# Kernel optimization log

Hardware: AMD Instinct MI355X
Metric: run time of the kernel (lower is better)

Reference implementation:

```python
import jax, jax.numpy as jnp
import numpy as np

N, T, H, L, E, F, CN, CG = 20000, 2, 128, 4, 320000, 514, 3, 2
EPS = 1e-7  # GENConv message epsilon


def _ln(x, g, b):
    mu = jnp.mean(x, axis=-1, keepdims=True)
    var = jnp.mean((x - mu) ** 2, axis=-1, keepdims=True)
    return (x - mu) / jnp.sqrt(var + 1e-5) * g + b


def _genconv(x, src, dst, e, W1, b1, g1, be1, W2, b2, t, n):
    # message: relu(x_j + edge_attr) + eps
    msg = jax.nn.relu(x[src] + e) + EPS  # [E,H]
    # softmax aggregation with learnable temperature t, grouped by dst
    logits = msg * t
    m = jax.ops.segment_max(logits, dst, num_segments=n)
    m = jnp.where(jnp.isfinite(m), m, 0.0)  # guard empty segments
    ex = jnp.exp(logits - m[dst])
    denom = jax.ops.segment_sum(ex, dst, num_segments=n)
    alpha = ex / (denom[dst] + 1e-16)
    agg = jax.ops.segment_sum(msg * alpha, dst, num_segments=n)  # [N,H]
    out = agg + x  # residual with root node (x_r)
    # MLP: Lin(H,2H) -> LayerNorm -> ReLU -> Lin(2H,H)
    h1 = jax.nn.relu(_ln(out @ W1 + b1, g1, be1))
    return h1 @ W2 + b2


def _attn(x, Wq, Wk, Wv, gamma):
    # x: [N, T, H]; channel (transform-axis) self-attention, gamma-gated residual
    q = jnp.einsum('tc,nch->nth', Wq, x)
    k = jnp.einsum('tc,nch->nth', Wk, x)
    v = jnp.einsum('tc,nch->nth', Wv, x)
    a = jax.nn.softmax(jnp.einsum('nth,nsh->nts', q, k), axis=-1)
    o = jnp.einsum('nts,nsh->nth', a, v)
    return gamma * o + x


def setup_inputs() -> dict:
    key = jax.random.key(0)
    ks = iter(jax.random.split(key, 48))

    def nrm(sh, s=0.02):
        return jax.random.normal(next(ks), sh, dtype=jnp.float32) * s

    inp = {}
    inp['node_feature'] = jax.random.normal(next(ks), (N, F), dtype=jnp.float32)
    inp['edge_index'] = jax.random.randint(next(ks), (T, 2, E), 0, N, dtype=jnp.int32)
    inp['edge_attr'] = jax.random.normal(next(ks), (T, E, 2), dtype=jnp.float32)
    # encoders
    inp['Wne'] = nrm((F, H)); inp['bne'] = jnp.zeros((H,), jnp.float32)
    inp['Wee'] = nrm((2, H)); inp['bee'] = jnp.zeros((H,), jnp.float32)
    # per-layer GENConv MLP params (stacked over L)
    inp['W1'] = nrm((L, H, 2 * H)); inp['b1'] = jnp.zeros((L, 2 * H), jnp.float32)
    inp['g1'] = jnp.ones((L, 2 * H), jnp.float32); inp['be1'] = jnp.zeros((L, 2 * H), jnp.float32)
    inp['W2'] = nrm((L, 2 * H, H)); inp['b2'] = jnp.zeros((L, H), jnp.float32)
    # DeepGCNLayer LayerNorms
    inp['dg'] = jnp.ones((L, H), jnp.float32); inp['db'] = jnp.zeros((L, H), jnp.float32)
    # learnable temperatures
    inp['t'] = jnp.ones((L,), jnp.float32)
    # node attention + head
    inp['Wq_n'] = nrm((T, T), 0.2); inp['Wk_n'] = nrm((T, T), 0.2); inp['Wv_n'] = nrm((T, T), 0.2)
    inp['gamma_n'] = jnp.float32(0.5)
    inp['Wn1'] = nrm((T * H, T * H)); inp['bn1'] = jnp.zeros((T * H,), jnp.float32)
    inp['Wn2'] = nrm((T * H, CN)); inp['bn2'] = jnp.zeros((CN,), jnp.float32)
    # graph attention + head
    inp['Wq_g'] = nrm((T, T), 0.2); inp['Wk_g'] = nrm((T, T), 0.2); inp['Wv_g'] = nrm((T, T), 0.2)
    inp['gamma_g'] = jnp.float32(0.5)
    inp['Wg1'] = nrm((T * H, T * H)); inp['bg1'] = jnp.zeros((T * H,), jnp.float32)
    inp['Wg2'] = nrm((T * H, CG)); inp['bg2'] = jnp.zeros((CG,), jnp.float32)
    return inp


def reference(node_feature, edge_index, edge_attr, Wne, bne, Wee, bee,
              W1, b1, g1, be1, W2, b2, dg, db, t,
              Wq_n, Wk_n, Wv_n, gamma_n, Wn1, bn1, Wn2, bn2,
              Wq_g, Wk_g, Wv_g, gamma_g, Wg1, bg1, Wg2, bg2):
    embs = []
    for ti in range(T):
        x = node_feature @ Wne + bne           # node_encoder
        e = edge_attr[ti] @ Wee + bee          # edge_encoder
        src, dst = edge_index[ti, 0], edge_index[ti, 1]
        # layers[0].conv applied directly
        x = _genconv(x, src, dst, e, W1[0], b1[0], g1[0], be1[0], W2[0], b2[0], t[0], N)
        # res+ DeepGCN blocks
        for l in range(1, L):
            h = jax.nn.relu(_ln(x, dg[l], db[l]))  # dropout p=0.1 is identity in eval
            x = x + _genconv(h, src, dst, e, W1[l], b1[l], g1[l], be1[l], W2[l], b2[l], t[l], N)
        x = jax.nn.relu(_ln(x, dg[0], db[0]))
        embs.append(x)
    emb = jnp.stack(embs, axis=1)  # [N, T, H]

    a = _attn(emb, Wq_n, Wk_n, Wv_n, gamma_n).reshape(N, T * H)
    node = jax.nn.relu(a @ Wn1 + bn1) @ Wn2 + bn2
    node = jax.nn.log_softmax(node, axis=-1)

    g = _attn(emb, Wq_g, Wk_g, Wv_g, gamma_g).reshape(N, T * H)
    gp = jnp.mean(g, axis=0, keepdims=True)  # global_mean_pool (single graph)
    gp = jax.nn.relu(gp @ Wg1 + bg1) @ Wg2 + bg2
    gp = jax.nn.log_softmax(gp, axis=-1)
    return (node, gp)
```

## Files before the change

### kernel.cpp

```cpp
#include <hip/hip_runtime.h>

#define NN 20000
#define TT 2
#define HH 128
#define LL 4
#define EE 320000
#define FF 514
#define CN 3
#define CG 2
#define MP 20096

typedef __bf16 bf16x8 __attribute__((ext_vector_type(8)));
typedef __bf16 bf16x4 __attribute__((ext_vector_type(4)));
typedef __bf16 bf16x2 __attribute__((ext_vector_type(2)));
typedef float f32x4 __attribute__((ext_vector_type(4)));

struct __align__(8) Edge { int src; __bf16 ea0, ea1; };

__device__ inline float wave_sum(float v) {
#pragma unroll
  for (int off = 32; off; off >>= 1) v += __shfl_xor(v, off);
  return v;
}
__device__ inline float red16(float v) {
  v += __shfl_xor(v, 1); v += __shfl_xor(v, 2);
  v += __shfl_xor(v, 4); v += __shfl_xor(v, 8);
  return v;
}

__device__ __forceinline__ float fexp2(float x) {
#if __has_builtin(__builtin_amdgcn_exp2f)
  return __builtin_amdgcn_exp2f(x);
#else
  return exp2f(x);
#endif
}

__device__ __forceinline__ void gload_lds16(const void* g, void* l) {
  __builtin_amdgcn_global_load_lds(
      (const __attribute__((address_space(1))) unsigned int*)g,
      (__attribute__((address_space(3))) unsigned int*)l, 16, 0, 0);
}

#define ENCB (MP / 64)
#define SSB 313
#define CHUNK 5000
__global__ __launch_bounds__(256) void enc_scatter_kernel(
    const __bf16* __restrict__ A, const __bf16* __restrict__ BT,
    const float* __restrict__ bias, __bf16* __restrict__ C,
    const int* __restrict__ edge_index, const float* __restrict__ edge_attr,
    int* __restrict__ cursor, Edge* __restrict__ edges) {
  __shared__ __bf16 As[2][64][32];
  __shared__ __bf16 Bs[2][128][32];
  const int tid = threadIdx.x;
  if (blockIdx.x >= ENCB) {
    int sb = blockIdx.x - ENCB;
    int chunk = sb & 7;
    int slice = sb >> 3;
    int i0 = slice * 2048 + tid * 8;
    if (i0 >= 2 * EE) return;
    int ti = (i0 >= EE) ? 1 : 0;
    int e0 = i0 - ti * EE;
    const int* srcp = edge_index + (size_t)ti * 2 * EE;
    int dst8[8];
    __builtin_memcpy(dst8, srcp + EE + e0, 32);
#pragma unroll
    for (int j = 0; j < 8; ++j) {
      int gnode = ti * NN + dst8[j];
      if (gnode / CHUNK != chunk) continue;
      int s = srcp[e0 + j];
      float2 ea = ((const float2*)edge_attr)[(size_t)ti * EE + e0 + j];
      int pos = atomicAdd(&cursor[gnode], 1);
      Edge ed;
      ed.src = s + ti * MP;
      ed.ea0 = (__bf16)ea.x; ed.ea1 = (__bf16)ea.y;
      __builtin_memcpy(&edges[pos], &ed, sizeof(Edge));
    }
    return;
  }
  const int K = 576;
  const int lane = tid & 63, w = tid >> 6;
  const int bm = blockIdx.x * 64;
  const int wr = (w >> 1) * 32, wc = (w & 1) * 64;
  const int fr = lane & 15, fq = lane >> 4;
  const int rowA = tid >> 2, chA = (tid & 3) * 8;
  const __bf16* Ab = A + (size_t)(bm + rowA) * K + chA;
  const __bf16* Bb = BT + (size_t)rowA * K + chA;
  const __bf16* Bb2 = Bb + (size_t)64 * K;
  f32x4 acc[2][4] = {};
#define STAGE(buf, k0)                                  \
  do {                                                  \
    gload_lds16(Ab + (k0), &As[buf][rowA][chA]);        \
    gload_lds16(Bb + (k0), &Bs[buf][rowA][chA]);        \
    gload_lds16(Bb2 + (k0), &Bs[buf][rowA + 64][chA]);  \
  } while (0)
  STAGE(0, 0);
  __syncthreads();
  int cur = 0;
  for (int k0 = 0; k0 < K; k0 += 32) {
    if (k0 + 32 < K) STAGE(cur ^ 1, k0 + 32);
    bf16x8 af[2], bq[4];
#pragma unroll
    for (int m = 0; m < 2; ++m)
      af[m] = *(const bf16x8*)&As[cur][wr + m * 16 + fr][fq * 8];
#pragma unroll
    for (int n = 0; n < 4; ++n)
      bq[n] = *(const bf16x8*)&Bs[cur][wc + n * 16 + fr][fq * 8];
#pragma unroll
    for (int m = 0; m < 2; ++m)
#pragma unroll
      for (int n = 0; n < 4; ++n)
        acc[m][n] =
            __builtin_amdgcn_mfma_f32_16x16x32_bf16(af[m], bq[n], acc[m][n], 0, 0, 0);
    __syncthreads();
    cur ^= 1;
  }
#undef STAGE
#pragma unroll
  for (int m = 0; m < 2; ++m) {
#pragma unroll
    for (int n = 0; n < 4; ++n) {
#pragma unroll
      for (int j = 0; j < 4; ++j) {
        int gm = bm + wr + m * 16 + fq * 4 + j;
        int gn = wc + n * 16 + fr;
        if (gm < NN) {
          __bf16 c = (__bf16)(acc[m][n][j] + bias[gn]);
          C[(size_t)gm * 128 + gn] = c;
          C[(size_t)(gm + MP) * 128 + gn] = c;
        }
      }
    }
  }
}

template <int EPI>
__global__ __launch_bounds__(256) void gemm256(
    const __bf16* __restrict__ A, const __bf16* __restrict__ BT,
    const float* __restrict__ bias, const float* __restrict__ g,
    const float* __restrict__ be, const float* __restrict__ W2h,
    const float* __restrict__ b2h, void* __restrict__ outp, int M, int K) {
  __shared__ __bf16 As[2][64][32];
  __shared__ __bf16 Bs[2][256][32];
  const int tid = threadIdx.x;
  const int lane = tid & 63, w = tid >> 6;
  const int bm = blockIdx.x * 64;
  const int wr = w * 16;
  const int fr = lane & 15, fq = lane >> 4;
  const int rowA = tid >> 2, chA = (tid & 3) * 8;
  const __bf16* Ab = A + (size_t)(bm + rowA) * K + chA;
  const __bf16* Bb = BT + (size_t)rowA * K + chA;
  f32x4 acc[16] = {};

#define STG(buf, k0)                                                \
  do {                                                              \
    gload_lds16(Ab + (k0), &As[buf][rowA][chA]);                    \
    _Pragma("unroll") for (int r = 0; r < 4; ++r)                   \
        gload_lds16(Bb + (size_t)(r * 64) * K + (k0),               \
                    &Bs[buf][rowA + r * 64][chA]);                  \
  } while (0)

  STG(0, 0);
  __syncthreads();
  int cur = 0;
  for (int k0 = 0; k0 < K; k0 += 32) {
    if (k0 + 32 < K) STG(cur ^ 1, k0 + 32);
    bf16x8 af = *(const bf16x8*)&As[cur][wr + fr][fq * 8];
#pragma unroll
    for (int n = 0; n < 16; ++n) {
      bf16x8 bq = *(const bf16x8*)&Bs[cur][n * 16 + fr][fq * 8];
      acc[n] = __builtin_amdgcn_mfma_f32_16x16x32_bf16(af, bq, acc[n], 0, 0, 0);
    }
    __syncthreads();
    cur ^= 1;
  }
#undef STG

  float cb[16];
#pragma unroll
  for (int n = 0; n < 16; ++n) cb[n] = bias[n * 16 + fr];

  if constexpr (EPI == 0) {
    float gv[16], bev[16];
#pragma unroll
    for (int n = 0; n < 16; ++n) {
      gv[n] = g[n * 16 + fr];
      bev[n] = be[n * 16 + fr];
    }
    __bf16* outb = (__bf16*)outp;
#pragma unroll
    for (int j = 0; j < 4; ++j) {
      float cj[16], s = 0.f, s2 = 0.f;
#pragma unroll
      for (int n = 0; n < 16; ++n) {
        float c = acc[n][j] + cb[n];
        cj[n] = c; s += c; s2 += c * c;
      }
      s = red16(s); s2 = red16(s2);
      float mu = s * (1.f / 256);
      float var = fmaxf(s2 * (1.f / 256) - mu * mu, 0.f);
      float rr = rsqrtf(var + 1e-5f);
      int gm = bm + wr + fq * 4 + j;
      __bf16* op = outb + (size_t)gm * 256;
#pragma unroll
      for (int n = 0; n < 16; ++n) {
        float y = (cj[n] - mu) * rr * gv[n] + bev[n];
        op[n * 16 + fr] = (__bf16)fmaxf(y, 0.f);
      }
    }
  } else {
    float w0[16], w1[16], w2[16];
#pragma unroll
    for (int n = 0; n < 16; ++n) {
      int col = n * 16 + fr;
      w0[n] = W2h[col * 3 + 0];
      w1[n] = W2h[col * 3 + 1];
      w2[n] = W2h[col * 3 + 2];
    }
    float* outf = (float*)outp;
#pragma unroll
    for (int j = 0; j < 4; ++j) {
      float p0 = 0.f, p1 = 0.f, p2 = 0.f;
#pragma unroll
      for (int n = 0; n < 16; ++n) {
        float h = fmaxf(acc[n][j] + cb[n], 0.f);
        p0 += h * w0[n]; p1 += h * w1[n]; p2 += h * w2[n];
      }
      p0 = red16(p0); p1 = red16(p1); p2 = red16(p2);
      int gm = bm + wr + fq * 4 + j;
      if (fr == 0 && gm < M) {
        float l0 = p0 + b2h[0], l1 = p1 + b2h[1], l2 = p2 + b2h[2];
        float m = fmaxf(l0, fmaxf(l1, l2));
        float lse = m + logf(__expf(l0 - m) + __expf(l1 - m) + __expf(l2 - m));
        outf[(size_t)gm * 3 + 0] = l0 - lse;
        outf[(size_t)gm * 3 + 1] = l1 - lse;
        outf[(size_t)gm * 3 + 2] = l2 - lse;
      }
    }
  }
}

template <int MODE>
__global__ __launch_bounds__(256) void gemm_lin2(
    const __bf16* __restrict__ A, const __bf16* __restrict__ BT,
    const float* __restrict__ bias, float* __restrict__ xres,
    const float* __restrict__ g, const float* __restrict__ be,
    void* __restrict__ lnout) {
  __shared__ __bf16 As[2][64][32];
  __shared__ __bf16 Bs[2][128][32];
  __shared__ float redS[64][2], redS2[64][2];
  const int tid = threadIdx.x;
  const int lane = tid & 63, w = tid >> 6;
  const int bm = blockIdx.x * 64;
  const int wr = (w >> 1) * 32, wc = (w & 1) * 64;
  const int fr = lane & 15, fq = lane >> 4;
  const int rowA = tid >> 2, chA = (tid & 3) * 8;
  const __bf16* Ab = A + (size_t)(bm + rowA) * 256 + chA;
  const __bf16* Bb = BT + (size_t)rowA * 256 + chA;
  const __bf16* Bb2 = Bb + (size_t)64 * 256;
  f32x4 acc[2][4] = {};

#define STAGE(buf, k0)                                  \
  do {                                                  \
    gload_lds16(Ab + (k0), &As[buf][rowA][chA]);        \
    gload_lds16(Bb + (k0), &Bs[buf][rowA][chA]);        \
    gload_lds16(Bb2 + (k0), &Bs[buf][rowA + 64][chA]);  \
  } while (0)

  STAGE(0, 0);
  __syncthreads();
  int cur = 0;
  for (int k0 = 0; k0 < 256; k0 += 32) {
    if (k0 + 32 < 256) STAGE(cur ^ 1, k0 + 32);
    bf16x8 af[2], bq[4];
#pragma unroll
    for (int m = 0; m < 2; ++m)
      af[m] = *(const bf16x8*)&As[cur][wr + m * 16 + fr][fq * 8];
#pragma unroll
    for (int n = 0; n < 4; ++n)
      bq[n] = *(const bf16x8*)&Bs[cur][wc + n * 16 + fr][fq * 8];
#pragma unroll
    for (int m = 0; m < 2; ++m)
#pragma unroll
      for (int n = 0; n < 4; ++n)
        acc[m][n] =
            __builtin_amdgcn_mfma_f32_16x16x32_bf16(af[m], bq[n], acc[m][n], 0, 0, 0);
    __syncthreads();
    cur ^= 1;
  }
#undef STAGE

  float cv[2][4][4];
#pragma unroll
  for (int m = 0; m < 2; ++m) {
    int r0 = wr + m * 16 + fq * 4;
#pragma unroll
    for (int j = 0; j < 4; ++j) {
      int gm = bm + r0 + j;
      float s = 0.f, s2 = 0.f;
#pragma unroll
      for (int n = 0; n < 4; ++n) {
        float c = acc[m][n][j] + bias[wc + n * 16 + fr];
        if (MODE != 0) c += xres[(size_t)gm * 128 + wc + n * 16 + fr];
        cv[m][n][j] = c;
        s += c; s2 += c * c;
      }
      s = red16(s); s2 = red16(s2);
      if (fr == 0) {
        redS[r0 + j][w & 1] = s;
        redS2[r0 + j][w & 1] = s2;
      }
    }
  }
  __syncthreads();
#pragma unroll
  for (int m = 0; m < 2; ++m) {
    int r0 = wr + m * 16 + fq * 4;
#pragma unroll
    for (int j = 0; j < 4; ++j) {
      int r = r0 + j;
      int gm = bm + r;
      float S = redS[r][0] + redS[r][1];
      float S2 = redS2[r][0] + redS2[r][1];
      float mu = S * (1.f / 128);
      float var = fmaxf(S2 * (1.f / 128) - mu * mu, 0.f);
      float rr = rsqrtf(var + 1e-5f);
      if constexpr (MODE < 2) {
        float* xp = xres + (size_t)gm * 128;
        __bf16* hp = (__bf16*)lnout + (size_t)gm * 128;
#pragma unroll
        for (int n = 0; n < 4; ++n) {
          int col = wc + n * 16 + fr;
          float c = cv[m][n][j];
          xp[col] = c;
          float y = (c - mu) * rr * g[col] + be[col];
          hp[col] = (__bf16)fmaxf(y, 0.f);
        }
      } else {
        int half = gm >= MP;
        int node = gm - half * MP;
        if (node < NN) {
          float* ep = (float*)lnout + (size_t)node * 256 + half * 128;
#pragma unroll
          for (int n = 0; n < 4; ++n) {
            int col = wc + n * 16 + fr;
            float y = (cv[m][n][j] - mu) * rr * g[col] + be[col];
            ep[col] = fmaxf(y, 0.f);
          }
        }
      }
    }
  }
}

struct WtDesc { const float* src; __bf16* dst; int K, N, Kpad, gbase; };
struct WtDescs { WtDesc d[10]; };
#define NFG 1440000
#define WTG 50176
#define CTG 80000
#define PREPG 2048

__global__ __launch_bounds__(256) void prep_kernel(
    const float* __restrict__ nf_src, __bf16* __restrict__ nf_dst, WtDescs descs,
    const int* __restrict__ edge_index, int* __restrict__ deg,
    float* __restrict__ gp_sum) {
  const int tid = threadIdx.x;
  if (blockIdx.x == 0) gp_sum[tid] = 0.f;
  const int TOT = NFG + WTG + CTG;
  for (int g = blockIdx.x * 256 + tid; g < TOT; g += PREPG * 256) {
    if (g < NFG) {
      int row = g / 72, colg = g - row * 72;
      int col0 = colg * 8;
      bf16x8 o;
      if (col0 + 8 <= FF) {
        float v[8];
        __builtin_memcpy(v, nf_src + (size_t)row * FF + col0, 32);
#pragma unroll
        for (int i = 0; i < 8; ++i) o[i] = (__bf16)v[i];
      } else {
#pragma unroll
        for (int i = 0; i < 8; ++i) {
          int col = col0 + i;
          o[i] = (__bf16)((col < FF) ? nf_src[(size_t)row * FF + col] : 0.f);
        }
      }
      *(bf16x8*)(nf_dst + (size_t)row * 576 + col0) = o;
    } else if (g < NFG + WTG) {
      int wb = g - NFG;
      int di = 0;
#pragma unroll
      for (int t = 1; t < 10; ++t)
        if (wb >= descs.d[t].gbase) di = t;
      WtDesc de = descs.d[di];
      int local = wb - de.gbase;
      int kg8 = de.Kpad >> 3;
      int n = local / kg8, k0 = (local - n * kg8) * 8;
      bf16x8 o;
#pragma unroll
      for (int i = 0; i < 8; ++i) {
        int k = k0 + i;
        o[i] = (__bf16)((k < de.K) ? de.src[(size_t)k * de.N + n] : 0.f);
      }
      *(bf16x8*)(de.dst + (size_t)n * de.Kpad + k0) = o;
    } else {
      int i0 = (g - NFG - WTG) * 8;
      int ti = (i0 >= EE) ? 1 : 0;
      int e0 = i0 - ti * EE;
      int dst8[8];
      __builtin_memcpy(dst8, edge_index + (size_t)ti * 2 * EE + EE + e0, 32);
      int* dbase = deg + ti * NN;
#pragma unroll
      for (int j = 0; j < 8; ++j) atomicAdd(&dbase[dst8[j]], 1);
    }
  }
}

__global__ __launch_bounds__(1024) void scan2_kernel(
    const int* __restrict__ deg_all, int* __restrict__ rowptr,
    int* __restrict__ cursor) {
  const int ti = blockIdx.x;
  const int* deg = deg_all + ti * NN;
  __shared__ int sums[1024];
  int tid = threadIdx.x;
  int chunk = (NN + 1023) / 1024;
  int begin = tid * chunk, end = min(begin + chunk, NN);
  int s = 0;
  for (int i = begin; i < end; ++i) s += deg[i];
  sums[tid] = s;
  __syncthreads();
  for (int off = 1; off < 1024; off <<= 1) {
    int v = (tid >= off) ? sums[tid - off] : 0;
    __syncthreads();
    sums[tid] += v;
    __syncthreads();
  }
  int running = ti * EE + sums[tid] - s;
  for (int i = begin; i < end; ++i) {
    rowptr[ti * NN + i] = running;
    cursor[ti * NN + i] = running;
    running += deg[i];
  }
  if (tid == 0 && ti == 1) rowptr[2 * NN] = 2 * EE;
}

__global__ __launch_bounds__(256) void agg_kernel(
    const __bf16* __restrict__ xin, const int* __restrict__ rowptr,
    const Edge* __restrict__ edges, const float* __restrict__ Wee,
    const float* __restrict__ bee, const float* __restrict__ tptr, int layer,
    __bf16* __restrict__ out) {
  int wave = threadIdx.x >> 6, lane = threadIdx.x & 63;
  int b = blockIdx.x;
  int x8 = b & 7;
  int q = x8 >> 1;
  int par = x8 & 1;
  int ti = q >> 1, chh = q & 1;
  int group = (b >> 3) * 2 + par;
  int qq = lane >> 4, c15 = lane & 15;
  int node = group * 16 + wave * 4 + qq;
  int gnode = ti * NN + node;
  int xrow = ti * MP + node;
  float t2 = tptr[layer] * 1.4426950408889634f;
  int c0 = chh * 64 + c15 * 4;
  float den[4] = {}, num[4] = {};
  int e = rowptr[gnode];
  const int e1 = rowptr[gnode + 1];

  if (t2 > 0.f) {
    float w0p[4], w1p[4], bvp[4];
#pragma unroll
    for (int i = 0; i < 4; ++i) {
      w0p[i] = Wee[c0 + i] * t2;
      w1p[i] = Wee[HH + c0 + i] * t2;
      bvp[i] = bee[c0 + i] * t2;
    }
#define MLPF(XV, ED)                                                      \
  do {                                                                    \
    float eax = (float)(ED).ea0, eay = (float)(ED).ea1;                   \
    _Pragma("unroll") for (int i = 0; i < 4; ++i) {                       \
      float te = fmaf(eax, w0p[i], fmaf(eay, w1p[i], bvp[i]));            \
      float sm = fmaxf(fmaf((float)(XV)[i], t2, te), 0.f);                \
      float ex = fexp2(sm);                                               \
      den[i] += ex; num[i] = fmaf(sm, ex, num[i]);                        \
    }                                                                     \
  } while (0)
    for (; e + 2 <= e1; e += 2) {
      Edge E0 = edges[e];
      Edge E1 = edges[e + 1];
      bf16x4 x0 = *(const bf16x4*)(xin + (size_t)E0.src * HH + c0);
      bf16x4 x1 = *(const bf16x4*)(xin + (size_t)E1.src * HH + c0);
      MLPF(x0, E0);
      MLPF(x1, E1);
    }
    if (e < e1) {
      Edge E0 = edges[e];
      bf16x4 x0 = *(const bf16x4*)(xin + (size_t)E0.src * HH + c0);
      MLPF(x0, E0);
    }
#undef MLPF
    bf16x4 xr = *(const bf16x4*)(xin + (size_t)xrow * HH + c0);
    bf16x4 o;
#pragma unroll
    for (int i = 0; i < 4; ++i)
      o[i] = (__bf16)(num[i] / (t2 * (den[i] + 1e-16f)) + (float)xr[i]);
    *(bf16x4*)(out + (size_t)xrow * HH + c0) = o;
  } else {
    float w0[4], w1[4], bv[4];
#pragma unroll
    for (int i = 0; i < 4; ++i) {
      w0[i] = Wee[c0 + i];
      w1[i] = Wee[HH + c0 + i];
      bv[i] = bee[c0 + i];
    }
    for (; e < e1; ++e) {
      Edge E0 = edges[e];
      bf16x4 xv = *(const bf16x4*)(xin + (size_t)E0.src * HH + c0);
      float eax = (float)E0.ea0, eay = (float)E0.ea1;
#pragma unroll
      for (int i = 0; i < 4; ++i) {
        float m =
            fmaxf((float)xv[i] + eax * w0[i] + eay * w1[i] + bv[i], 0.f) + 1e-7f;
        float ex = fexp2(m * t2);
        den[i] += ex; num[i] += m * ex;
      }
    }
    bf16x4 xr = *(const bf16x4*)(xin + (size_t)xrow * HH + c0);
    bf16x4 o;
#pragma unroll
    for (int i = 0; i < 4; ++i)
      o[i] = (__bf16)(num[i] / (den[i] + 1e-16f) + (float)xr[i]);
    *(bf16x4*)(out + (size_t)xrow * HH + c0) = o;
  }
}

__global__ __launch_bounds__(256) void attn2_kernel(
    const float* __restrict__ emb, const float* __restrict__ Wq_n,
    const float* __restrict__ Wk_n, const float* __restrict__ Wv_n,
    const float* __restrict__ gn, const float* __restrict__ Wq_g,
    const float* __restrict__ Wk_g, const float* __restrict__ Wv_g,
    const float* __restrict__ gg, __bf16* __restrict__ outn,
    float* __restrict__ partial) {
  __shared__ float gsum[4][256];
  int wave = threadIdx.x >> 6, lane = threadIdx.x & 63;
  int tid = threadIdx.x;
  int n = blockIdx.x * 4 + wave;
  int c0 = lane * 2;
  const float* base = emb + (size_t)n * (2 * HH);
  float2 x0 = *(const float2*)(base + c0);
  float2 x1 = *(const float2*)(base + HH + c0);

#define ATTN_BODY(Wq, Wk, Wv, GAM, O0A, O0B, O1A, O1B)                        \
  {                                                                           \
    float gamma = *(GAM);                                                     \
    float wq00 = Wq[0], wq01 = Wq[1], wq10 = Wq[2], wq11 = Wq[3];             \
    float wk00 = Wk[0], wk01 = Wk[1], wk10 = Wk[2], wk11 = Wk[3];             \
    float wv00 = Wv[0], wv01 = Wv[1], wv10 = Wv[2], wv11 = Wv[3];             \
    float q0a = wq00 * x0.x + wq01 * x1.x, q0b = wq00 * x0.y + wq01 * x1.y;   \
    float q1a = wq10 * x0.x + wq11 * x1.x, q1b = wq10 * x0.y + wq11 * x1.y;   \
    float k0a = wk00 * x0.x + wk01 * x1.x, k0b = wk00 * x0.y + wk01 * x1.y;   \
    float k1a = wk10 * x0.x + wk11 * x1.x, k1b = wk10 * x0.y + wk11 * x1.y;   \
    float v0a = wv00 * x0.x + wv01 * x1.x, v0b = wv00 * x0.y + wv01 * x1.y;   \
    float v1a = wv10 * x0.x + wv11 * x1.x, v1b = wv10 * x0.y + wv11 * x1.y;   \
    float s00 = wave_sum(q0a * k0a + q0b * k0b);                              \
    float s01 = wave_sum(q0a * k1a + q0b * k1b);                              \
    float s10 = wave_sum(q1a * k0a + q1b * k0b);                              \
    float s11 = wave_sum(q1a * k1a + q1b * k1b);                              \
    float m0 = fmaxf(s00, s01);                                               \
    float e00 = __expf(s00 - m0), e01 = __expf(s01 - m0);                     \
    float i0 = 1.f / (e00 + e01);                                             \
    float a00 = e00 * i0, a01 = e01 * i0;                                     \
    float m1 = fmaxf(s10, s11);                                               \
    float e10 = __expf(s10 - m1), e11 = __expf(s11 - m1);                     \
    float i1 = 1.f / (e10 + e11);                                             \
    float a10 = e10 * i1, a11 = e11 * i1;                                     \
    O0A = gamma * (a00 * v0a + a01 * v1a) + x0.x;                             \
    O0B = gamma * (a00 * v0b + a01 * v1b) + x0.y;                             \
    O1A = gamma * (a10 * v0a + a11 * v1a) + x1.x;                             \
    O1B = gamma * (a10 * v0b + a11 * v1b) + x1.y;                             \
  }

  float n0a, n0b, n1a, n1b;
  ATTN_BODY(Wq_n, Wk_n, Wv_n, gn, n0a, n0b, n1a, n1b);
  __bf16* opn = outn + (size_t)n * (2 * HH);
  bf16x2 t0; t0[0] = (__bf16)n0a; t0[1] = (__bf16)n0b;
  bf16x2 t1; t1[0] = (__bf16)n1a; t1[1] = (__bf16)n1b;
  *(bf16x2*)(opn + c0) = t0;
  *(bf16x2*)(opn + HH + c0) = t1;

  float g0a, g0b, g1a, g1b;
  ATTN_BODY(Wq_g, Wk_g, Wv_g, gg, g0a, g0b, g1a, g1b);
  gsum[wave][c0] = g0a;
  gsum[wave][c0 + 1] = g0b;
  gsum[wave][128 + c0] = g1a;
  gsum[wave][129 + c0] = g1b;
  __syncthreads();
  partial[(size_t)blockIdx.x * 256 + tid] =
      gsum[0][tid] + gsum[1][tid] + gsum[2][tid] + gsum[3][tid];
#undef ATTN_BODY
}

__global__ __launch_bounds__(256) void pool_kernel(const float* __restrict__ partial,
                                                   float* __restrict__ gp_sum,
                                                   int nRows) {
  int c = threadIdx.x;
  float s = 0.f;
  for (int r = blockIdx.x; r < nRows; r += gridDim.x)
    s += partial[(size_t)r * 256 + c];
  atomicAdd(&gp_sum[c], s);
}

__global__ __launch_bounds__(256) void graph_head_kernel(
    const float* __restrict__ gp_sum, const float* __restrict__ Wg1,
    const float* __restrict__ bg1, const float* __restrict__ Wg2,
    const float* __restrict__ bg2, float* __restrict__ outp, float invN) {
  __shared__ float gp[256];
  __shared__ float h1[256];
  __shared__ float lg[2];
  int tid = threadIdx.x;
  gp[tid] = gp_sum[tid] * invN;
  __syncthreads();
  float acc = bg1[tid];
  for (int k = 0; k < 256; ++k) acc += gp[k] * Wg1[k * 256 + tid];
  h1[tid] = fmaxf(acc, 0.f);
  __syncthreads();
  if (tid < 2) {
    float l = bg2[tid];
    for (int c = 0; c < 256; ++c) l += h1[c] * Wg2[c * 2 + tid];
    lg[tid] = l;
  }
  __syncthreads();
  if (tid == 0) {
    float m = fmaxf(lg[0], lg[1]);
    float lse = m + logf(__expf(lg[0] - m) + __expf(lg[1] - m));
    outp[0] = lg[0] - lse;
    outp[1] = lg[1] - lse;
  }
}

extern "C" void kernel_launch(void* const* d_in, const int* in_sizes, int n_in,
                              void* d_out, int out_size, void* d_ws, size_t ws_size,
                              hipStream_t stream) {
  (void)in_sizes; (void)n_in; (void)out_size; (void)ws_size;
  const float* node_feature = (const float*)d_in[0];
  const int* edge_index = (const int*)d_in[1];
  const float* edge_attr = (const float*)d_in[2];
  const float* Wne = (const float*)d_in[3];
  const float* bne = (const float*)d_in[4];
  const float* Wee = (const float*)d_in[5];
  const float* bee = (const float*)d_in[6];
  const float* W1 = (const float*)d_in[7];
  const float* b1 = (const float*)d_in[8];
  const float* g1 = (const float*)d_in[9];
  const float* be1 = (const float*)d_in[10];
  const float* W2 = (const float*)d_in[11];
  const float* b2 = (const float*)d_in[12];
  const float* dg = (const float*)d_in[13];
  const float* db = (const float*)d_in[14];
  const float* tpar = (const float*)d_in[15];
  const float* Wq_n = (const float*)d_in[16];
  const float* Wk_n = (const float*)d_in[17];
  const float* Wv_n = (const float*)d_in[18];
  const float* gamma_n = (const float*)d_in[19];
  const float* Wn1 = (const float*)d_in[20];
  const float* bn1 = (const float*)d_in[21];
  const float* Wn2 = (const float*)d_in[22];
  const float* bn2 = (const float*)d_in[23];
  const float* Wq_g = (const float*)d_in[24];
  const float* Wk_g = (const float*)d_in[25];
  const float* Wv_g = (const float*)d_in[26];
  const float* gamma_g = (const float*)d_in[27];
  const float* Wg1 = (const float*)d_in[28];
  const float* bg1 = (const float*)d_in[29];
  const float* Wg2 = (const float*)d_in[30];
  const float* bg2 = (const float*)d_in[31];
  float* out = (float*)d_out;

  char* pc = (char*)d_ws;
  auto alloc = [&](size_t bytes) {
    char* r = pc;
    pc += (bytes + 255) & ~(size_t)255;
    return r;
  };
  float* xbuf = (float*)alloc((size_t)2 * MP * HH * 4);
  __bf16* hbuf_b = (__bf16*)alloc((size_t)2 * MP * HH * 2);
  __bf16* t256_b = (__bf16*)alloc((size_t)2 * MP * 256 * 2);
  float* emb = (float*)alloc((size_t)NN * 2 * HH * 4);
  __bf16* aggout_b = (__bf16*)alloc((size_t)2 * MP * HH * 2);
  __bf16* nf_b = (__bf16*)emb;
  __bf16* attnb = t256_b;
  float* partial = xbuf;
  __bf16* wt_ne = (__bf16*)alloc((size_t)128 * 576 * 2);
  __bf16* wt1 = (__bf16*)alloc((size_t)4 * 256 * 128 * 2);
  __bf16* wt2 = (__bf16*)alloc((size_t)4 * 128 * 256 * 2);
  __bf16* wtn1 = (__bf16*)alloc((size_t)256 * 256 * 2);
  float* gp_sum = (float*)alloc(256 * 4);
  int* deg = (int*)alloc((size_t)2 * NN * 4);
  int* cursor = (int*)alloc((size_t)2 * NN * 4);
  int* rowptr = (int*)alloc((size_t)(2 * NN + 2) * 4);
  Edge* edges = (Edge*)alloc((size_t)2 * EE * 8);

  const int gRows2 = 2 * MP / 64;

  WtDescs wd;
  int gb = 0;
  wd.d[0] = {Wne, wt_ne, FF, HH, 576, gb}; gb += HH * 576 / 8;
  for (int l = 0; l < 4; ++l) {
    wd.d[1 + l] = {W1 + (size_t)l * HH * 256, wt1 + (size_t)l * 256 * HH, HH, 256,
                   HH, gb};
    gb += 256 * HH / 8;
  }
  for (int l = 0; l < 4; ++l) {
    wd.d[5 + l] = {W2 + (size_t)l * 256 * HH, wt2 + (size_t)l * HH * 256, 256, HH,
                   256, gb};
    gb += HH * 256 / 8;
  }
  wd.d[9] = {Wn1, wtn1, 256, 256, 256, gb};

  hipMemsetAsync(deg, 0, 2 * NN * sizeof(int), stream);
  prep_kernel<<<PREPG, 256, 0, stream>>>(node_feature, nf_b, wd, edge_index, deg,
                                         gp_sum);
  scan2_kernel<<<2, 1024, 0, stream>>>(deg, rowptr, cursor);
  enc_scatter_kernel<<<ENCB + 8 * SSB, 256, 0, stream>>>(
      nf_b, wt_ne, bne, hbuf_b, edge_index, edge_attr, cursor, edges);

  for (int l = 0; l < LL; ++l) {
    agg_kernel<<<625 * 8, 256, 0, stream>>>(hbuf_b, rowptr, edges, Wee, bee, tpar,
                                            l, aggout_b);
    gemm256<0><<<gRows2, 256, 0, stream>>>(aggout_b, wt1 + (size_t)l * 256 * HH,
                                           b1 + l * 2 * HH, g1 + l * 2 * HH,
                                           be1 + l * 2 * HH, nullptr, nullptr, t256_b,
                                           2 * MP, HH);
    const __bf16* w2l = wt2 + (size_t)l * HH * 256;
    const float* b2l = b2 + l * HH;
    if (l == 0)
      gemm_lin2<0><<<gRows2, 256, 0, stream>>>(t256_b, w2l, b2l, xbuf, dg + 1 * HH,
                                               db + 1 * HH, hbuf_b);
    else if (l < LL - 1)
      gemm_lin2<1><<<gRows2, 256, 0, stream>>>(t256_b, w2l, b2l, xbuf,
                                               dg + (l + 1) * HH, db + (l + 1) * HH,
                                               hbuf_b);
    else
      gemm_lin2<2><<<gRows2, 256, 0, stream>>>(t256_b, w2l, b2l, xbuf, dg, db, emb);
  }

  attn2_kernel<<<NN / 4, 256, 0, stream>>>(emb, Wq_n, Wk_n, Wv_n, gamma_n, Wq_g,
                                           Wk_g, Wv_g, gamma_g, attnb, partial);
  gemm256<1><<<MP / 64, 256, 0, stream>>>(attnb, wtn1, bn1, nullptr, nullptr, Wn2,
                                          bn2, out, NN, 256);
  pool_kernel<<<128, 256, 0, stream>>>(partial, gp_sum, NN / 4);
  graph_head_kernel<<<1, 256, 0, stream>>>(gp_sum, Wg1, bg1, Wg2, bg2,
                                           out + (size_t)NN * CN, 1.0f / NN);
}
```

Before: 442.5 us.

## Fuse GENConv MLP lin1+LayerNorm and lin2 GEMMs into one kernel via LDS

Merges the first MLP GEMM (with its LayerNorm/ReLU epilogue) and the second GEMM into one kernel per layer. The 64x256 bf16 hidden tile stays in shared memory and feeds the second GEMM directly, so the large global intermediate buffer and one launch per layer go away. Shared memory per block grows substantially, which may reduce occupancy. The head GEMM is split out as a standalone non-templated kernel.

```diff
diff --git a/kernel.cpp b/kernel.cpp
--- a/kernel.cpp
+++ b/kernel.cpp
@@ -134,12 +134,10 @@
   }
 }
 
-template <int EPI>
-__global__ __launch_bounds__(256) void gemm256(
+__global__ __launch_bounds__(256) void gemm256_head(
     const __bf16* __restrict__ A, const __bf16* __restrict__ BT,
-    const float* __restrict__ bias, const float* __restrict__ g,
-    const float* __restrict__ be, const float* __restrict__ W2h,
-    const float* __restrict__ b2h, void* __restrict__ outp, int M, int K) {
+    const float* __restrict__ bias, const float* __restrict__ W2h,
+    const float* __restrict__ b2h, float* __restrict__ outf, int M, int K) {
   __shared__ __bf16 As[2][64][32];
   __shared__ __bf16 Bs[2][256][32];
   const int tid = threadIdx.x;
@@ -176,18 +174,89 @@
   }
 #undef STG
 
-  float cb[16];
-#pragma unroll
-  for (int n = 0; n < 16; ++n) cb[n] = bias[n * 16 + fr];
-
-  if constexpr (EPI == 0) {
-    float gv[16], bev[16];
+  float cb[16], w0[16], w1[16], w2[16];
+#pragma unroll
+  for (int n = 0; n < 16; ++n) {
+    int col = n * 16 + fr;
+    cb[n] = bias[col];
+    w0[n] = W2h[col * 3 + 0];
+    w1[n] = W2h[col * 3 + 1];
+    w2[n] = W2h[col * 3 + 2];
+  }
+#pragma unroll
+  for (int j = 0; j < 4; ++j) {
+    float p0 = 0.f, p1 = 0.f, p2 = 0.f;
 #pragma unroll
     for (int n = 0; n < 16; ++n) {
-      gv[n] = g[n * 16 + fr];
-      bev[n] = be[n * 16 + fr];
-    }
-    __bf16* outb = (__bf16*)outp;
+      float h = fmaxf(acc[n][j] + cb[n], 0.f);
+      p0 += h * w0[n]; p1 += h * w1[n]; p2 += h * w2[n];
+    }
+    p0 = red16(p0); p1 = red16(p1); p2 = red16(p2);
+    int gm = bm + wr + fq * 4 + j;
+    if (fr == 0 && gm < M) {
+      float l0 = p0 + b2h[0], l1 = p1 + b2h[1], l2 = p2 + b2h[2];
+      float m = fmaxf(l0, fmaxf(l1, l2));
+      float lse = m + logf(__expf(l0 - m) + __expf(l1 - m) + __expf(l2 - m));
+      outf[(size_t)gm * 3 + 0] = l0 - lse;
+      outf[(size_t)gm * 3 + 1] = l1 - lse;
+      outf[(size_t)gm * 3 + 2] = l2 - lse;
+    }
+  }
+}
+
+template <int MODE>
+__global__ __launch_bounds__(256) void gemm_layer(
+    const __bf16* __restrict__ A, const __bf16* __restrict__ W1T,
+    const float* __restrict__ b1, const float* __restrict__ g1,
+    const float* __restrict__ be1, const __bf16* __restrict__ W2T,
+    const float* __restrict__ b2, float* __restrict__ xres,
+    const float* __restrict__ dgv, const float* __restrict__ dbv,
+    void* __restrict__ lnout) {
+  __shared__ char smem[40960];
+  __shared__ __bf16 h1[64][264];
+  __shared__ float redS[64][2], redS2[64][2];
+  auto As = (__bf16(*)[64][32])smem;
+  auto Bs1 = (__bf16(*)[256][32])(smem + 8192);
+  auto Bs2 = (__bf16(*)[128][32])smem;
+  const int tid = threadIdx.x;
+  const int lane = tid & 63, w = tid >> 6;
+  const int bm = blockIdx.x * 64;
+  const int fr = lane & 15, fq = lane >> 4;
+  const int rowA = tid >> 2, chA = (tid & 3) * 8;
+
+  {
+    const int wr = w * 16;
+    const __bf16* Ab = A + (size_t)(bm + rowA) * 128 + chA;
+    const __bf16* Bb = W1T + (size_t)rowA * 128 + chA;
+    f32x4 acc[16] = {};
+#define STG1(buf, k0)                                                 \
+  do {                                                                \
+    gload_lds16(Ab + (k0), &As[buf][rowA][chA]);                      \
+    _Pragma("unroll") for (int r = 0; r < 4; ++r)                     \
+        gload_lds16(Bb + (size_t)(r * 64) * 128 + (k0),               \
+                    &Bs1[buf][rowA + r * 64][chA]);                   \
+  } while (0)
+    STG1(0, 0);
+    __syncthreads();
+    int cur = 0;
+    for (int k0 = 0; k0 < 128; k0 += 32) {
+      if (k0 + 32 < 128) STG1(cur ^ 1, k0 + 32);
+      bf16x8 af = *(const bf16x8*)&As[cur][wr + fr][fq * 8];
+#pragma unroll
+      for (int n = 0; n < 16; ++n) {
+        bf16x8 bq = *(const bf16x8*)&Bs1[cur][n * 16 + fr][fq * 8];
+        acc[n] = __builtin_amdgcn_mfma_f32_16x16x32_bf16(af, bq, acc[n], 0, 0, 0);
+      }
+      __syncthreads();
+      cur ^= 1;
+    }
+#undef STG1
+    float cb[16], gv[16], bev[16];
+#pragma unroll
+    for (int n = 0; n < 16; ++n) {
+      int col = n * 16 + fr;
+      cb[n] = b1[col]; gv[n] = g1[col]; bev[n] = be1[col];
+    }
 #pragma unroll
     for (int j = 0; j < 4; ++j) {
       float cj[16], s = 0.f, s2 = 0.f;
@@ -200,152 +269,106 @@
       float mu = s * (1.f / 256);
       float var = fmaxf(s2 * (1.f / 256) - mu * mu, 0.f);
       float rr = rsqrtf(var + 1e-5f);
-      int gm = bm + wr + fq * 4 + j;
-      __bf16* op = outb + (size_t)gm * 256;
+      int r = wr + fq * 4 + j;
 #pragma unroll
       for (int n = 0; n < 16; ++n) {
         float y = (cj[n] - mu) * rr * gv[n] + bev[n];
-        op[n * 16 + fr] = (__bf16)fmaxf(y, 0.f);
-      }
-    }
-  } else {
-    float w0[16], w1[16], w2[16];
-#pragma unroll
-    for (int n = 0; n < 16; ++n) {
-      int col = n * 16 + fr;
-      w0[n] = W2h[col * 3 + 0];
-      w1[n] = W2h[col * 3 + 1];
-      w2[n] = W2h[col * 3 + 2];
-    }
-    float* outf = (float*)outp;
-#pragma unroll
-    for (int j = 0; j < 4; ++j) {
-      float p0 = 0.f, p1 = 0.f, p2 = 0.f;
-#pragma unroll
-      for (int n = 0; n < 16; ++n) {
-        float h = fmaxf(acc[n][j] + cb[n], 0.f);
-        p0 += h * w0[n]; p1 += h * w1[n]; p2 += h * w2[n];
-      }
-      p0 = red16(p0); p1 = red16(p1); p2 = red16(p2);
-      int gm = bm + wr + fq * 4 + j;
-      if (fr == 0 && gm < M) {
-        float l0 = p0 + b2h[0], l1 = p1 + b2h[1], l2 = p2 + b2h[2];
-        float m = fmaxf(l0, fmaxf(l1, l2));
-        float lse = m + logf(__expf(l0 - m) + __expf(l1 - m) + __expf(l2 - m));
-        outf[(size_t)gm * 3 + 0] = l0 - lse;
-        outf[(size_t)gm * 3 + 1] = l1 - lse;
-        outf[(size_t)gm * 3 + 2] = l2 - lse;
-      }
-    }
-  }
-}
-
-template <int MODE>
-__global__ __launch_bounds__(256) void gemm_lin2(
-    const __bf16* __restrict__ A, const __bf16* __restrict__ BT,
-    const float* __restrict__ bias, float* __restrict__ xres,
-    const float* __restrict__ g, const float* __restrict__ be,
-    void* __restrict__ lnout) {
-  __shared__ __bf16 As[2][64][32];
-  __shared__ __bf16 Bs[2][128][32];
-  __shared__ float redS[64][2], redS2[64][2];
-  const int tid = threadIdx.x;
-  const int lane = tid & 63, w = tid >> 6;
-  const int bm = blockIdx.x * 64;
-  const int wr = (w >> 1) * 32, wc = (w & 1) * 64;
-  const int fr = lane & 15, fq = lane >> 4;
-  const int rowA = tid >> 2, chA = (tid & 3) * 8;
-  const __bf16* Ab = A + (size_t)(bm + rowA) * 256 + chA;
-  const __bf16* Bb = BT + (size_t)rowA * 256 + chA;
-  const __bf16* Bb2 = Bb + (size_t)64 * 256;
-  f32x4 acc[2][4] = {};
-
-#define STAGE(buf, k0)                                  \
+        h1[r][n * 16 + fr] = (__bf16)fmaxf(y, 0.f);
+      }
+    }
+  }
+  __syncthreads();
+
+  {
+    const int wr = (w >> 1) * 32, wc = (w & 1) * 64;
+    const __bf16* Bb = W2T + (size_t)rowA * 256 + chA;
+    const __bf16* Bb2 = Bb + (size_t)64 * 256;
+    f32x4 acc[2][4] = {};
+#define STG2(buf, k0)                                   \
   do {                                                  \
-    gload_lds16(Ab + (k0), &As[buf][rowA][chA]);        \
-    gload_lds16(Bb + (k0), &Bs[buf][rowA][chA]);        \
-    gload_lds16(Bb2 + (k0), &Bs[buf][rowA + 64][chA]);  \
+    gload_lds16(Bb + (k0), &Bs2[buf][rowA][chA]);       \
+    gload_lds16(Bb2 + (k0), &Bs2[buf][rowA + 64][chA]); \
   } while (0)
-
-  STAGE(0, 0);
-  __syncthreads();
-  int cur = 0;
-  for (int k0 = 0; k0 < 256; k0 += 32) {
-    if (k0 + 32 < 256) STAGE(cur ^ 1, k0 + 32);
-    bf16x8 af[2], bq[4];
-#pragma unroll
-    for (int m = 0; m < 2; ++m)
-      af[m] = *(const bf16x8*)&As[cur][wr + m * 16 + fr][fq * 8];
-#pragma unroll
-    for (int n = 0; n < 4; ++n)
-      bq[n] = *(const bf16x8*)&Bs[cur][wc + n * 16 + fr][fq * 8];
-#pragma unroll
-    for (int m = 0; m < 2; ++m)
+    STG2(0, 0);
+    __syncthreads();
+    int cur = 0;
+    for (int k0 = 0; k0 < 256; k0 += 32) {
+      if (k0 + 32 < 256) STG2(cur ^ 1, k0 + 32);
+      bf16x8 af[2], bq[4];
+#pragma unroll
+      for (int m = 0; m < 2; ++m)
+        af[m] = *(const bf16x8*)&h1[wr + m * 16 + fr][k0 + fq * 8];
 #pragma unroll
       for (int n = 0; n < 4; ++n)
-        acc[m][n] =
-            __builtin_amdgcn_mfma_f32_16x16x32_bf16(af[m], bq[n], acc[m][n], 0, 0, 0);
+        bq[n] = *(const bf16x8*)&Bs2[cur][wc + n * 16 + fr][fq * 8];
+#pragma unroll
+      for (int m = 0; m < 2; ++m)
+#pragma unroll
+        for (int n = 0; n < 4; ++n)
+          acc[m][n] =
+              __builtin_amdgcn_mfma_f32_16x16x32_bf16(af[m], bq[n], acc[m][n], 0, 0, 0);
+      __syncthreads();
+      cur ^= 1;
+    }
+#undef STG2
+
+    float cv[2][4][4];
+#pragma unroll
+    for (int m = 0; m < 2; ++m) {
+      int r0 = wr + m * 16 + fq * 4;
+#pragma unroll
+      for (int j = 0; j < 4; ++j) {
+        int gm = bm + r0 + j;
+        float s = 0.f, s2 = 0.f;
+#pragma unroll
+        for (int n = 0; n < 4; ++n) {
+          float c = acc[m][n][j] + b2[wc + n * 16 + fr];
+          if (MODE != 0) c += xres[(size_t)gm * 128 + wc + n * 16 + fr];
+          cv[m][n][j] = c;
+          s += c; s2 += c * c;
+        }
+        s = red16(s); s2 = red16(s2);
+        if (fr == 0) {
+          redS[r0 + j][w & 1] = s;
+          redS2[r0 + j][w & 1] = s2;
+        }
+      }
+    }
     __syncthreads();
-    cur ^= 1;
-  }
-#undef STAGE
-
-  float cv[2][4][4];
-#pragma unroll
-  for (int m = 0; m < 2; ++m) {
-    int r0 = wr + m * 16 + fq * 4;
-#pragma unroll
-    for (int j = 0; j < 4; ++j) {
-      int gm = bm + r0 + j;
-      float s = 0.f, s2 = 0.f;
-#pragma unroll
-      for (int n = 0; n < 4; ++n) {
-        float c = acc[m][n][j] + bias[wc + n * 16 + fr];
-        if (MODE != 0) c += xres[(size_t)gm * 128 + wc + n * 16 + fr];
-        cv[m][n][j] = c;
-        s += c; s2 += c * c;
-      }
-      s = red16(s); s2 = red16(s2);
-      if (fr == 0) {
-        redS[r0 + j][w & 1] = s;
-        redS2[r0 + j][w & 1] = s2;
-      }
-    }
-  }
-  __syncthreads();
-#pragma unroll
-  for (int m = 0; m < 2; ++m) {
-    int r0 = wr + m * 16 + fq * 4;
-#pragma unroll
-    for (int j = 0; j < 4; ++j) {
-      int r = r0 + j;
-      int gm = bm + r;
-      float S = redS[r][0] + redS[r][1];
-      float S2 = redS2[r][0] + redS2[r][1];
-      float mu = S * (1.f / 128);
-      float var = fmaxf(S2 * (1.f / 128) - mu * mu, 0.f);
-      float rr = rsqrtf(var + 1e-5f);
-      if constexpr (MODE < 2) {
-        float* xp = xres + (size_t)gm * 128;
-        __bf16* hp = (__bf16*)lnout + (size_t)gm * 128;
-#pragma unroll
-        for (int n = 0; n < 4; ++n) {
-          int col = wc + n * 16 + fr;
-          float c = cv[m][n][j];
-          xp[col] = c;
-          float y = (c - mu) * rr * g[col] + be[col];
-          hp[col] = (__bf16)fmaxf(y, 0.f);
-        }
-      } else {
-        int half = gm >= MP;
-        int node = gm - half * MP;
-        if (node < NN) {
-          float* ep = (float*)lnout + (size_t)node * 256 + half * 128;
+#pragma unroll
+    for (int m = 0; m < 2; ++m) {
+      int r0 = wr + m * 16 + fq * 4;
+#pragma unroll
+      for (int j = 0; j < 4; ++j) {
+        int r = r0 + j;
+        int gm = bm + r;
+        float S = redS[r][0] + redS[r][1];
+        float S2 = redS2[r][0] + redS2[r][1];
+        float mu = S * (1.f / 128);
+        float var = fmaxf(S2 * (1.f / 128) - mu * mu, 0.f);
+        float rr = rsqrtf(var + 1e-5f);
+        if constexpr (MODE < 2) {
+          float* xp = xres + (size_t)gm * 128;
+          __bf16* hp = (__bf16*)lnout + (size_t)gm * 128;
 #pragma unroll
           for (int n = 0; n < 4; ++n) {
             int col = wc + n * 16 + fr;
-            float y = (cv[m][n][j] - mu) * rr * g[col] + be[col];
-            ep[col] = fmaxf(y, 0.f);
+            float c = cv[m][n][j];
+            xp[col] = c;
+            float y = (c - mu) * rr * dgv[col] + dbv[col];
+            hp[col] = (__bf16)fmaxf(y, 0.f);
+          }
+        } else {
+          int half = gm >= MP;
+          int node = gm - half * MP;
+          if (node < NN) {
+            float* ep = (float*)lnout + (size_t)node * 256 + half * 128;
+#pragma unroll
+            for (int n = 0; n < 4; ++n) {
+              int col = wc + n * 16 + fr;
+              float y = (cv[m][n][j] - mu) * rr * dgv[col] + dbv[col];
+              ep[col] = fmaxf(y, 0.f);
+            }
           }
         }
       }
@@ -682,11 +705,10 @@
   };
   float* xbuf = (float*)alloc((size_t)2 * MP * HH * 4);
   __bf16* hbuf_b = (__bf16*)alloc((size_t)2 * MP * HH * 2);
-  __bf16* t256_b = (__bf16*)alloc((size_t)2 * MP * 256 * 2);
+  __bf16* attnb = (__bf16*)alloc((size_t)MP * 256 * 2);
   float* emb = (float*)alloc((size_t)NN * 2 * HH * 4);
   __bf16* aggout_b = (__bf16*)alloc((size_t)2 * MP * HH * 2);
   __bf16* nf_b = (__bf16*)emb;
-  __bf16* attnb = t256_b;
   float* partial = xbuf;
   __bf16* wt_ne = (__bf16*)alloc((size_t)128 * 576 * 2);
   __bf16* wt1 = (__bf16*)alloc((size_t)4 * 256 * 128 * 2);
@@ -725,27 +747,26 @@
   for (int l = 0; l < LL; ++l) {
     agg_kernel<<<625 * 8, 256, 0, stream>>>(hbuf_b, rowptr, edges, Wee, bee, tpar,
                                             l, aggout_b);
-    gemm256<0><<<gRows2, 256, 0, stream>>>(aggout_b, wt1 + (size_t)l * 256 * HH,
-                                           b1 + l * 2 * HH, g1 + l * 2 * HH,
-                                           be1 + l * 2 * HH, nullptr, nullptr, t256_b,
-                                           2 * MP, HH);
+    const __bf16* w1l = wt1 + (size_t)l * 256 * HH;
     const __bf16* w2l = wt2 + (size_t)l * HH * 256;
-    const float* b2l = b2 + l * HH;
     if (l == 0)
-      gemm_lin2<0><<<gRows2, 256, 0, stream>>>(t256_b, w2l, b2l, xbuf, dg + 1 * HH,
-                                               db + 1 * HH, hbuf_b);
+      gemm_layer<0><<<gRows2, 256, 0, stream>>>(
+          aggout_b, w1l, b1 + l * 2 * HH, g1 + l * 2 * HH, be1 + l * 2 * HH, w2l,
+          b2 + l * HH, xbuf, dg + 1 * HH, db + 1 * HH, hbuf_b);
     else if (l < LL - 1)
-      gemm_lin2<1><<<gRows2, 256, 0, stream>>>(t256_b, w2l, b2l, xbuf,
-                                               dg + (l + 1) * HH, db + (l + 1) * HH,
-                                               hbuf_b);
+      gemm_layer<1><<<gRows2, 256, 0, stream>>>(
+          aggout_b, w1l, b1 + l * 2 * HH, g1 + l * 2 * HH, be1 + l * 2 * HH, w2l,
+          b2 + l * HH, xbuf, dg + (l + 1) * HH, db + (l + 1) * HH, hbuf_b);
     else
-      gemm_lin2<2><<<gRows2, 256, 0, stream>>>(t256_b, w2l, b2l, xbuf, dg, db, emb);
+      gemm_layer<2><<<gRows2, 256, 0, stream>>>(
+          aggout_b, w1l, b1 + l * 2 * HH, g1 + l * 2 * HH, be1 + l * 2 * HH, w2l,
+          b2 + l * HH, xbuf, dg, db, emb);
   }
 
   attn2_kernel<<<NN / 4, 256, 0, stream>>>(emb, Wq_n, Wk_n, Wv_n, gamma_n, Wq_g,
                                            Wk_g, Wv_g, gamma_g, attnb, partial);
-  gemm256<1><<<MP / 64, 256, 0, stream>>>(attnb, wtn1, bn1, nullptr, nullptr, Wn2,
-                                          bn2, out, NN, 256);
+  gemm256_head<<<MP / 64, 256, 0, stream>>>(attnb, wtn1, bn1, Wn2, bn2, out, NN,
+                                            256);
   pool_kernel<<<128, 256, 0, stream>>>(partial, gp_sum, NN / 4);
   graph_head_kernel<<<1, 256, 0, stream>>>(gp_sum, Wg1, bg1, Wg2, bg2,
                                            out + (size_t)NN * CN, 1.0f / NN);
```

Result: faster. 433.4 us (-2.0%).
